# Performance work log

Measured on AMD Instinct MI355X. Metric: run time of the kernel, lower is better.

Reference implementation:

```python
import jax, jax.numpy as jnp
import numpy as np

DIM = 512
NUM_HEAD = 8
HEAD_DIM = DIM // NUM_HEAD
FFN = 4 * DIM


def setup_inputs() -> dict:
    key = jax.random.key(0)
    ks = jax.random.split(key, 16)
    s = DIM ** -0.5
    inp = {
        "x": jax.random.normal(ks[0], (4, 2048, DIM), jnp.float32),
        "wq": jax.random.normal(ks[1], (DIM, DIM), jnp.float32) * s,
        "bq": jnp.zeros((DIM,), jnp.float32),
        "wk": jax.random.normal(ks[2], (DIM, DIM), jnp.float32) * s,
        "bk": jnp.zeros((DIM,), jnp.float32),
        "wv": jax.random.normal(ks[3], (DIM, DIM), jnp.float32) * s,
        "bv": jnp.zeros((DIM,), jnp.float32),
        "wo": jax.random.normal(ks[4], (DIM, DIM), jnp.float32) * s,
        "bo": jnp.zeros((DIM,), jnp.float32),
        "w1": jax.random.normal(ks[5], (DIM, FFN), jnp.float32) * s,
        "b1": jnp.zeros((FFN,), jnp.float32),
        "w2": jax.random.normal(ks[6], (FFN, DIM), jnp.float32) * (FFN ** -0.5),
        "b2": jnp.zeros((DIM,), jnp.float32),
        "g1": jnp.ones((DIM,), jnp.float32),
        "be1": jnp.zeros((DIM,), jnp.float32),
        "g2": jnp.ones((DIM,), jnp.float32),
        "be2": jnp.zeros((DIM,), jnp.float32),
    }
    return inp


def layer_norm(x, g, b, eps=1e-5):
    mu = jnp.mean(x, axis=-1, keepdims=True)
    var = jnp.var(x, axis=-1, keepdims=True)
    return (x - mu) * jax.lax.rsqrt(var + eps) * g + b


def _forward(x, wq, bq, wk, bk, wv, bv, wo, bo, w1, b1, w2, b2, g1, be1, g2, be2):
    b, n, _ = x.shape
    scale = HEAD_DIM ** -0.5
    q = (x @ wq + bq).reshape(b, n, NUM_HEAD, HEAD_DIM).transpose(0, 2, 1, 3)
    k = (x @ wk + bk).reshape(b, n, NUM_HEAD, HEAD_DIM).transpose(0, 2, 1, 3)
    v = (x @ wv + bv).reshape(b, n, NUM_HEAD, HEAD_DIM).transpose(0, 2, 1, 3)
    scores = jnp.einsum('bhqd,bhkd->bhqk', q, k) * scale
    attn = jax.nn.softmax(scores, axis=-1)
    out = jnp.einsum('bhqk,bhkd->bhqd', attn, v)
    out = out.transpose(0, 2, 1, 3).reshape(b, n, DIM)
    out = out @ wo + bo
    x = layer_norm(out + x, g1, be1)
    h = jax.nn.gelu(x @ w1 + b1, approximate=False)
    ff = h @ w2 + b2
    x = layer_norm(ff + x, g2, be2)
    return x


def reference(x, wq, bq, wk, bk, wv, bv, wo, bo, w1, b1, w2, b2, g1, be1, g2, be2):
    return _forward(x, wq, bq, wk, bk, wv, bv, wo, bo, w1, b1, w2, b2, g1, be1, g2, be2)
```

## Files before the change

kernel.cpp:

```cpp
#include <hip/hip_runtime.h>
#include <math.h>

#define DIM 512
#define NHEAD 8
#define HD 64
#define FFN_DIM 2048
#define BATCH 4
#define SEQ 2048
#define MTOK (BATCH*SEQ)

typedef __attribute__((ext_vector_type(8))) short bf16x8;
typedef __attribute__((ext_vector_type(4))) float f32x4;

__device__ __forceinline__ unsigned short f2b(float f){
    unsigned int u = __float_as_uint(f);
    u += 0x7fffu + ((u >> 16) & 1u);
    return (unsigned short)(u >> 16);
}
__device__ __forceinline__ float b2f(unsigned short u){
    return __uint_as_float(((unsigned int)u) << 16);
}
__device__ __forceinline__ unsigned int pack_trunc(float f0, float f1){
    return __builtin_amdgcn_perm(__float_as_uint(f1), __float_as_uint(f0), 0x07060302u);
}
__device__ __forceinline__ void async_cp16(const unsigned short* g, unsigned short* l){
    __builtin_amdgcn_global_load_lds((const __attribute__((address_space(1))) unsigned int*)g,
                                     (__attribute__((address_space(3))) unsigned int*)l, 16, 0, 0);
}

__device__ __forceinline__ void transp32(const float* __restrict__ in, unsigned short* __restrict__ out,
                                         int N, int K, int n0_rd, int n0_wr, int k0,
                                         unsigned short (&t)[32][33], int tid){
    int tx = tid & 31, ty = tid >> 5;
    #pragma unroll
    for (int u = 0; u < 4; u++)
        t[tx][ty + 8*u] = f2b(in[(size_t)(k0 + ty + 8*u)*N + n0_rd + tx]);
    __syncthreads();
    #pragma unroll
    for (int u = 0; u < 4; u++)
        out[(size_t)(n0_wr + ty + 8*u)*K + k0 + tx] = t[ty + 8*u][tx];
}

__global__ void prep_kernel(const float* __restrict__ x,
                            const float* __restrict__ wq, const float* __restrict__ wk,
                            const float* __restrict__ wv, const float* __restrict__ wo,
                            const float* __restrict__ w1, const float* __restrict__ w2,
                            const float* __restrict__ bq, const float* __restrict__ bk,
                            const float* __restrict__ bv,
                            unsigned short* __restrict__ xb, unsigned short* __restrict__ wqkvT,
                            unsigned short* __restrict__ woT, unsigned short* __restrict__ w1T,
                            unsigned short* __restrict__ w2T, float* __restrict__ bqkv)
{
    __shared__ unsigned short t[32][33];
    int bid = blockIdx.x, tid = threadIdx.x;
    if (bid < 4096) {
        int i = (bid*256 + tid)*4;
        float4 v = *(const float4*)(x + i);
        ushort4 o; o.x=f2b(v.x); o.y=f2b(v.y); o.z=f2b(v.z); o.w=f2b(v.w);
        *(ushort4*)(xb + i) = o;
    } else if (bid < 4864) {
        int r = bid - 4096;
        int n0 = (r % 48)*32, k0 = (r / 48)*32;
        const float* w = (n0 < 512) ? wq : (n0 < 1024) ? wk : wv;
        transp32(w, wqkvT, 512, 512, n0 & 511, n0, k0, t, tid);
    } else if (bid < 5120) {
        int r = bid - 4864;
        int n0 = (r % 16)*32, k0 = (r / 16)*32;
        transp32(wo, woT, 512, 512, n0, n0, k0, t, tid);
    } else if (bid < 6144) {
        int r = bid - 5120;
        int n0 = (r % 64)*32, k0 = (r / 64)*32;
        transp32(w1, w1T, 2048, 512, n0, n0, k0, t, tid);
    } else if (bid < 7168) {
        int r = bid - 6144;
        int n0 = (r % 16)*32, k0 = (r / 16)*32;
        transp32(w2, w2T, 512, 2048, n0, n0, k0, t, tid);
    } else {
        int i = (bid - 7168)*256 + tid;
        if (i < 1536)
            bqkv[i] = (i < 512) ? bq[i] : (i < 1024) ? bk[i-512] : bv[i-1024];
    }
}

template<int MODE, int TN, int SK>
__global__ __launch_bounds__(256)
void gemm_bf16(const unsigned short* __restrict__ A, const unsigned short* __restrict__ Bt,
               const float* __restrict__ bias,
               float* __restrict__ Cf, unsigned short* __restrict__ Cb,
               unsigned short* __restrict__ qo, unsigned short* __restrict__ ko,
               unsigned short* __restrict__ vTo,
               int M, int N, int K)
{
    constexpr int JN = (TN == 128) ? 4 : 2;
    __shared__ unsigned short As[128*64];
    __shared__ unsigned short Bs[TN*64];
    int tid  = threadIdx.x;
    int lane = tid & 63;
    int ln = lane & 15, qd = lane >> 4;
    int m0 = blockIdx.x * 128, n0 = blockIdx.y * TN;
    int wid = tid >> 6;
    int wm = (wid >> 1) * 64;
    int wn = (wid & 1) * (16*JN);
    int kbeg = (SK > 1) ? (int)blockIdx.z * (K/SK) : 0;
    int kend = kbeg + K/SK;
    if (SK > 1) Cf += (size_t)blockIdx.z * M * N;

    f32x4 acc[4][JN];
    #pragma unroll
    for (int i = 0; i < 4; i++)
        #pragma unroll
        for (int j = 0; j < JN; j++) acc[i][j] = (f32x4){0.f,0.f,0.f,0.f};

    for (int k0 = kbeg; k0 < kend; k0 += 64) {
        #pragma unroll
        for (int i = 0; i < 4; i++) {
            int cid = i*256 + tid;
            int row = cid >> 3, cs = cid & 7;
            int cg = cs ^ (row & 7);
            async_cp16(&A[(size_t)(m0+row)*K + k0 + cg*8], &As[(cid & ~63) * 8]);
        }
        #pragma unroll
        for (int i = 0; i < TN/32; i++) {
            int cid = i*256 + tid;
            int row = cid >> 3, cs = cid & 7;
            int cg = cs ^ (row & 7);
            async_cp16(&Bt[(size_t)(n0+row)*K + k0 + cg*8], &Bs[(cid & ~63) * 8]);
        }
        __syncthreads();
        #pragma unroll
        for (int kk = 0; kk < 64; kk += 32) {
            int c0 = kk >> 3;
            bf16x8 af[4], bf[JN];
            #pragma unroll
            for (int t = 0; t < 4; t++)
                af[t] = *(bf16x8*)&As[(wm + t*16 + ln)*64 + ((c0 + qd) ^ (ln & 7))*8];
            #pragma unroll
            for (int t = 0; t < JN; t++)
                bf[t] = *(bf16x8*)&Bs[(wn + t*16 + ln)*64 + ((c0 + qd) ^ (ln & 7))*8];
            #pragma unroll
            for (int i = 0; i < 4; i++)
                #pragma unroll
                for (int j = 0; j < JN; j++)
                    acc[i][j] = __builtin_amdgcn_mfma_f32_16x16x32_bf16(af[i], bf[j], acc[i][j], 0,0,0);
        }
        __syncthreads();
    }

    const float QSCALE = 0.18033688011112042f;
    #pragma unroll
    for (int i = 0; i < 4; i++) {
        int mb = m0 + wm + i*16 + qd*4;
        #pragma unroll
        for (int j = 0; j < JN; j++) {
            int c = n0 + wn + j*16 + ln;
            float bv_ = (SK > 1 && blockIdx.z) ? 0.f : bias[c];
            float v[4];
            #pragma unroll
            for (int r = 0; r < 4; r++) v[r] = acc[i][j][r] + bv_;
            if (MODE == 0) {
                #pragma unroll
                for (int r = 0; r < 4; r++) Cf[(size_t)(mb+r)*N + c] = v[r];
            } else if (MODE == 2) {
                #pragma unroll
                for (int r = 0; r < 4; r++) {
                    float g = 0.5f * v[r] * (1.0f + erff(v[r] * 0.70710678118654752f));
                    Cb[(size_t)(mb+r)*N + c] = f2b(g);
                }
            } else {
                int b = mb >> 11, t0 = mb & 2047;
                if (c < 512) {
                    int h = c >> 6, hd = c & 63;
                    #pragma unroll
                    for (int r = 0; r < 4; r++)
                        qo[(((size_t)(b*8 + h))*SEQ + t0 + r)*64 + hd] = f2b(v[r] * QSCALE);
                } else if (c < 1024) {
                    int cc = c - 512, h = cc >> 6, hd = cc & 63;
                    #pragma unroll
                    for (int r = 0; r < 4; r++)
                        ko[(((size_t)(b*8 + h))*SEQ + t0 + r)*64 + hd] = f2b(v[r]);
                } else {
                    int cc = c - 1024, h = cc >> 6, hd = cc & 63;
                    ushort4 pk;
                    pk.x = f2b(v[0]); pk.y = f2b(v[1]); pk.z = f2b(v[2]); pk.w = f2b(v[3]);
                    *(ushort4*)&vTo[(((size_t)(b*8 + h))*64 + hd)*SEQ + t0] = pk;
                }
            }
        }
    }
}

__global__ __launch_bounds__(256)
void attn_mfma(const unsigned short* __restrict__ Q, const unsigned short* __restrict__ K,
               const unsigned short* __restrict__ VT, unsigned short* __restrict__ O)
{
    __shared__ unsigned short lds[24576];
    unsigned short* Qs = lds + 8192;
    unsigned short* Ps = lds + 16384;
    int tid  = threadIdx.x;
    int wid  = tid >> 6, lane = tid & 63;
    int ln = lane & 15, qd = lane >> 4;
    int qb = blockIdx.x, bh = blockIdx.y;

    #pragma unroll
    for (int i = 0; i < 4; i++) {
        int cid = i*256 + tid;
        int row = cid >> 3, cs = cid & 7;
        int cg = cs ^ (row & 7);
        async_cp16(&Q[((size_t)bh*SEQ + qb*128 + row)*64 + cg*8], &Qs[(cid & ~63)*8]);
    }
    #pragma unroll
    for (int i = 0; i < 2; i++) {
        int cid = i*256 + tid;
        int row = cid >> 3, cs = cid & 7;
        int cg = cs ^ (row & 7);
        async_cp16(&K [((size_t)bh*SEQ + row)*64 + cg*8], &lds[(cid & ~63)*8]);
        async_cp16(&VT[((size_t)bh*64 + row)*SEQ + cg*8], &lds[4096 + (cid & ~63)*8]);
    }
    __syncthreads();

    bf16x8 qf[2][2];
    #pragma unroll
    for (int qs = 0; qs < 2; qs++)
        #pragma unroll
        for (int kk = 0; kk < 2; kk++)
            qf[qs][kk] = *(bf16x8*)&Qs[(wid*32 + qs*16 + ln)*64 + ((kk*4 + qd) ^ (ln & 7))*8];
    __syncthreads();

    f32x4 o[2][4];
    #pragma unroll
    for (int qs = 0; qs < 2; qs++)
        #pragma unroll
        for (int dt = 0; dt < 4; dt++) o[qs][dt] = (f32x4){0.f,0.f,0.f,0.f};
    float l_i[2] = {0.f, 0.f};

    for (int kt = 0; kt < 32; kt++) {
        int kof = (kt & 1) * 8192;
        int vof = 4096 + kof;
        if (kt < 31) {
            int nkof = 8192 - kof;
            #pragma unroll
            for (int i = 0; i < 2; i++) {
                int cid = i*256 + tid;
                int row = cid >> 3, cs = cid & 7;
                int cg = cs ^ (row & 7);
                async_cp16(&K [((size_t)bh*SEQ + (kt+1)*64 + row)*64 + cg*8], &lds[nkof + (cid & ~63)*8]);
                async_cp16(&VT[((size_t)bh*64 + row)*SEQ + (kt+1)*64 + cg*8], &lds[nkof + 4096 + (cid & ~63)*8]);
            }
        }

        f32x4 s[2][4];
        #pragma unroll
        for (int qs = 0; qs < 2; qs++)
            #pragma unroll
            for (int nt = 0; nt < 4; nt++) s[qs][nt] = (f32x4){0.f,0.f,0.f,0.f};
        #pragma unroll
        for (int kk = 0; kk < 2; kk++) {
            #pragma unroll
            for (int nt = 0; nt < 4; nt++) {
                bf16x8 kf = *(bf16x8*)&lds[kof + (nt*16 + ln)*64 + ((kk*4 + qd) ^ (ln & 7))*8];
                s[0][nt] = __builtin_amdgcn_mfma_f32_16x16x32_bf16(kf, qf[0][kk], s[0][nt], 0,0,0);
                s[1][nt] = __builtin_amdgcn_mfma_f32_16x16x32_bf16(kf, qf[1][kk], s[1][nt], 0,0,0);
            }
        }

        #pragma unroll
        for (int qs = 0; qs < 2; qs++) {
            #pragma unroll
            for (int nt = 0; nt < 4; nt++) {
                #pragma unroll
                for (int r = 0; r < 4; r++) {
                    float p = __builtin_amdgcn_exp2f(s[qs][nt][r]);
                    s[qs][nt][r] = p;
                    l_i[qs] += p;
                }
                uint2 pk;
                pk.x = pack_trunc(s[qs][nt][0], s[qs][nt][1]);
                pk.y = pack_trunc(s[qs][nt][2], s[qs][nt][3]);
                *(uint2*)&Ps[(wid*32 + qs*16 + ln)*64 + ((nt*2 + (qd>>1)) ^ (ln & 7))*8 + (qd&1)*4] = pk;
            }
        }

        #pragma unroll
        for (int kk = 0; kk < 2; kk++) {
            bf16x8 pf0 = *(bf16x8*)&Ps[(wid*32 + ln)*64      + ((kk*4 + qd) ^ (ln & 7))*8];
            bf16x8 pf1 = *(bf16x8*)&Ps[(wid*32 + 16 + ln)*64 + ((kk*4 + qd) ^ (ln & 7))*8];
            #pragma unroll
            for (int dt = 0; dt < 4; dt++) {
                bf16x8 vf = *(bf16x8*)&lds[vof + (dt*16 + ln)*64 + ((kk*4 + qd) ^ (ln & 7))*8];
                o[0][dt] = __builtin_amdgcn_mfma_f32_16x16x32_bf16(vf, pf0, o[0][dt], 0,0,0);
                o[1][dt] = __builtin_amdgcn_mfma_f32_16x16x32_bf16(vf, pf1, o[1][dt], 0,0,0);
            }
        }
        __syncthreads();
    }

    int b = bh >> 3, h = bh & 7;
    #pragma unroll
    for (int qs = 0; qs < 2; qs++) {
        float l = l_i[qs];
        l += __shfl_xor(l, 16);
        l += __shfl_xor(l, 32);
        float linv = 1.0f / l;
        int t = qb*128 + wid*32 + qs*16 + ln;
        #pragma unroll
        for (int dt = 0; dt < 4; dt++) {
            ushort4 pk;
            pk.x = f2b(o[qs][dt][0]*linv); pk.y = f2b(o[qs][dt][1]*linv);
            pk.z = f2b(o[qs][dt][2]*linv); pk.w = f2b(o[qs][dt][3]*linv);
            *(ushort4*)&O[((size_t)b*SEQ + t)*DIM + h*64 + dt*16 + qd*4] = pk;
        }
    }
}

__global__ void ln1_kernel(const float* __restrict__ m0p, const float* __restrict__ m1p,
                           const float* __restrict__ resp,
                           const float* __restrict__ g, const float* __restrict__ be,
                           unsigned short* __restrict__ outb)
{
    int row  = blockIdx.x*4 + (threadIdx.x >> 6);
    int lane = threadIdx.x & 63;
    size_t base = (size_t)row * DIM + lane*8;

    float4 a0 = *(const float4*)(m0p + base);
    float4 a1 = *(const float4*)(m0p + base + 4);
    float4 c0 = *(const float4*)(m1p + base);
    float4 c1 = *(const float4*)(m1p + base + 4);
    float4 r0 = *(const float4*)(resp + base);
    float4 r1 = *(const float4*)(resp + base + 4);
    float v[8] = { a0.x+c0.x+r0.x, a0.y+c0.y+r0.y, a0.z+c0.z+r0.z, a0.w+c0.w+r0.w,
                   a1.x+c1.x+r1.x, a1.y+c1.y+r1.y, a1.z+c1.z+r1.z, a1.w+c1.w+r1.w };
    float s = 0.f, s2 = 0.f;
    #pragma unroll
    for (int i = 0; i < 8; i++) { s += v[i]; s2 += v[i]*v[i]; }
    #pragma unroll
    for (int d = 32; d >= 1; d >>= 1) { s += __shfl_xor(s, d); s2 += __shfl_xor(s2, d); }
    float mean = s * (1.0f / DIM);
    float rstd = rsqrtf(s2 * (1.0f / DIM) - mean*mean + 1e-5f);

    float4 g0 = *(const float4*)(g + lane*8);
    float4 g1 = *(const float4*)(g + lane*8 + 4);
    float4 b0 = *(const float4*)(be + lane*8);
    float4 b1 = *(const float4*)(be + lane*8 + 4);
    float gg[8] = {g0.x,g0.y,g0.z,g0.w,g1.x,g1.y,g1.z,g1.w};
    float bb[8] = {b0.x,b0.y,b0.z,b0.w,b1.x,b1.y,b1.z,b1.w};
    ushort4 p0, p1;
    float o[8];
    #pragma unroll
    for (int i = 0; i < 8; i++) o[i] = (v[i]-mean)*rstd*gg[i] + bb[i];
    p0.x=f2b(o[0]); p0.y=f2b(o[1]); p0.z=f2b(o[2]); p0.w=f2b(o[3]);
    p1.x=f2b(o[4]); p1.y=f2b(o[5]); p1.z=f2b(o[6]); p1.w=f2b(o[7]);
    *(ushort4*)(outb + base)     = p0;
    *(ushort4*)(outb + base + 4) = p1;
}

__global__ void ln2_kernel(const float* __restrict__ m0p, const float* __restrict__ m1p,
                           const unsigned short* __restrict__ resb,
                           const float* __restrict__ g, const float* __restrict__ be,
                           float* __restrict__ outf)
{
    int row  = blockIdx.x*4 + (threadIdx.x >> 6);
    int lane = threadIdx.x & 63;
    size_t base = (size_t)row * DIM + lane*8;

    float4 a0 = *(const float4*)(m0p + base);
    float4 a1 = *(const float4*)(m0p + base + 4);
    float4 c0 = *(const float4*)(m1p + base);
    float4 c1 = *(const float4*)(m1p + base + 4);
    ushort4 rb0 = *(const ushort4*)(resb + base);
    ushort4 rb1 = *(const ushort4*)(resb + base + 4);
    float v[8] = { a0.x+c0.x+b2f(rb0.x), a0.y+c0.y+b2f(rb0.y),
                   a0.z+c0.z+b2f(rb0.z), a0.w+c0.w+b2f(rb0.w),
                   a1.x+c1.x+b2f(rb1.x), a1.y+c1.y+b2f(rb1.y),
                   a1.z+c1.z+b2f(rb1.z), a1.w+c1.w+b2f(rb1.w) };
    float s = 0.f, s2 = 0.f;
    #pragma unroll
    for (int i = 0; i < 8; i++) { s += v[i]; s2 += v[i]*v[i]; }
    #pragma unroll
    for (int d = 32; d >= 1; d >>= 1) { s += __shfl_xor(s, d); s2 += __shfl_xor(s2, d); }
    float mean = s * (1.0f / DIM);
    float rstd = rsqrtf(s2 * (1.0f / DIM) - mean*mean + 1e-5f);

    float4 g0 = *(const float4*)(g + lane*8);
    float4 g1 = *(const float4*)(g + lane*8 + 4);
    float4 b0 = *(const float4*)(be + lane*8);
    float4 b1 = *(const float4*)(be + lane*8 + 4);
    float gg[8] = {g0.x,g0.y,g0.z,g0.w,g1.x,g1.y,g1.z,g1.w};
    float bb[8] = {b0.x,b0.y,b0.z,b0.w,b1.x,b1.y,b1.z,b1.w};
    float o[8];
    #pragma unroll
    for (int i = 0; i < 8; i++) o[i] = (v[i] - mean)*rstd*gg[i] + bb[i];
    *(float4*)(outf + base)     = (float4){o[0],o[1],o[2],o[3]};
    *(float4*)(outf + base + 4) = (float4){o[4],o[5],o[6],o[7]};
}

extern "C" void kernel_launch(void* const* d_in, const int* in_sizes, int n_in,
                              void* d_out, int out_size, void* d_ws, size_t ws_size,
                              hipStream_t stream) {
    const float* x   = (const float*)d_in[0];
    const float* wq  = (const float*)d_in[1];
    const float* bq  = (const float*)d_in[2];
    const float* wk  = (const float*)d_in[3];
    const float* bk  = (const float*)d_in[4];
    const float* wv  = (const float*)d_in[5];
    const float* bv  = (const float*)d_in[6];
    const float* wo  = (const float*)d_in[7];
    const float* bo  = (const float*)d_in[8];
    const float* w1  = (const float*)d_in[9];
    const float* b1  = (const float*)d_in[10];
    const float* w2  = (const float*)d_in[11];
    const float* b2  = (const float*)d_in[12];
    const float* g1  = (const float*)d_in[13];
    const float* be1 = (const float*)d_in[14];
    const float* g2  = (const float*)d_in[15];
    const float* be2 = (const float*)d_in[16];
    float* out = (float*)d_out;

    char* w = (char*)d_ws;
    size_t off = 0;
    auto alloc = [&](size_t bytes){ void* p = w + off; off += (bytes + 255) & ~(size_t)255; return p; };
    unsigned short* xb     = (unsigned short*)alloc((size_t)MTOK*DIM*2);
    unsigned short* wqkvT  = (unsigned short*)alloc((size_t)1536*512*2);
    unsigned short* woT    = (unsigned short*)alloc((size_t)512*512*2);
    unsigned short* w1T    = (unsigned short*)alloc((size_t)2048*512*2);
    unsigned short* w2T    = (unsigned short*)alloc((size_t)512*2048*2);
    float*          bqkv   = (float*)alloc(1536*4);
    unsigned short* qb_    = (unsigned short*)alloc((size_t)32*SEQ*64*2);
    unsigned short* kb_    = (unsigned short*)alloc((size_t)32*SEQ*64*2);
    unsigned short* vT_    = (unsigned short*)alloc((size_t)32*64*SEQ*2);
    unsigned short* attno  = (unsigned short*)alloc((size_t)MTOK*DIM*2);
    unsigned short* x1b    = (unsigned short*)alloc((size_t)MTOK*DIM*2);
    unsigned short* h_     = (unsigned short*)alloc((size_t)MTOK*FFN_DIM*2);
    float*          ff     = (float*)alloc((size_t)2*MTOK*DIM*4);

    prep_kernel<<<7174, 256, 0, stream>>>(x, wq, wk, wv, wo, w1, w2, bq, bk, bv,
                                          xb, wqkvT, woT, w1T, w2T, bqkv);

    gemm_bf16<1,128,1><<<dim3(64,12), 256, 0, stream>>>(xb, wqkvT, bqkv, nullptr, nullptr,
                                                        qb_, kb_, vT_, MTOK, 1536, DIM);
    attn_mfma<<<dim3(16,32), 256, 0, stream>>>(qb_, kb_, vT_, attno);
    gemm_bf16<0,128,2><<<dim3(64,4,2), 256, 0, stream>>>(attno, woT, bo, ff, nullptr,
                                                         nullptr, nullptr, nullptr, MTOK, DIM, DIM);
    ln1_kernel<<<MTOK/4, 256, 0, stream>>>(ff, ff + (size_t)MTOK*DIM, x, g1, be1, x1b);
    gemm_bf16<2,128,1><<<dim3(64,16), 256, 0, stream>>>(x1b, w1T, b1, nullptr, h_,
                                                        nullptr, nullptr, nullptr, MTOK, FFN_DIM, DIM);
    gemm_bf16<0,128,2><<<dim3(64,4,2), 256, 0, stream>>>(h_, w2T, b2, ff, nullptr,
                                                         nullptr, nullptr, nullptr, MTOK, DIM, FFN_DIM);
    ln2_kernel<<<MTOK/4, 256, 0, stream>>>(ff, ff + (size_t)MTOK*DIM, x1b, g2, be2, out);
}
```

Measured before the change: 272.4 us.

## Use two-wave attention blocks with 64 rows per wave; bf16 split-K partials

Attention blocks now use 128 threads, each wave handling 64 query rows, so every K/V fragment read from LDS feeds twice as many MFMAs. The Q tile is staged in the P buffer region. Split-K GEMM partial outputs feeding the layer norms are stored in bf16 rather than fp32, halving that write/read traffic. This costs more registers per wave and adds bf16 rounding before the residual and layer norm.

```diff
diff --git a/kernel.cpp b/kernel.cpp
--- a/kernel.cpp
+++ b/kernel.cpp
@@ -86,7 +86,7 @@
 __global__ __launch_bounds__(256)
 void gemm_bf16(const unsigned short* __restrict__ A, const unsigned short* __restrict__ Bt,
                const float* __restrict__ bias,
-               float* __restrict__ Cf, unsigned short* __restrict__ Cb,
+               unsigned short* __restrict__ Cb,
                unsigned short* __restrict__ qo, unsigned short* __restrict__ ko,
                unsigned short* __restrict__ vTo,
                int M, int N, int K)
@@ -103,7 +103,7 @@
     int wn = (wid & 1) * (16*JN);
     int kbeg = (SK > 1) ? (int)blockIdx.z * (K/SK) : 0;
     int kend = kbeg + K/SK;
-    if (SK > 1) Cf += (size_t)blockIdx.z * M * N;
+    if (SK > 1 && MODE == 0) Cb += (size_t)blockIdx.z * M * N;
 
     f32x4 acc[4][JN];
     #pragma unroll
@@ -159,7 +159,7 @@
             for (int r = 0; r < 4; r++) v[r] = acc[i][j][r] + bv_;
             if (MODE == 0) {
                 #pragma unroll
-                for (int r = 0; r < 4; r++) Cf[(size_t)(mb+r)*N + c] = v[r];
+                for (int r = 0; r < 4; r++) Cb[(size_t)(mb+r)*N + c] = f2b(v[r]);
             } else if (MODE == 2) {
                 #pragma unroll
                 for (int r = 0; r < 4; r++) {
@@ -189,12 +189,11 @@
     }
 }
 
-__global__ __launch_bounds__(256)
+__global__ __launch_bounds__(128)
 void attn_mfma(const unsigned short* __restrict__ Q, const unsigned short* __restrict__ K,
                const unsigned short* __restrict__ VT, unsigned short* __restrict__ O)
 {
     __shared__ unsigned short lds[24576];
-    unsigned short* Qs = lds + 8192;
     unsigned short* Ps = lds + 16384;
     int tid  = threadIdx.x;
     int wid  = tid >> 6, lane = tid & 63;
@@ -202,15 +201,15 @@
     int qb = blockIdx.x, bh = blockIdx.y;
 
     #pragma unroll
-    for (int i = 0; i < 4; i++) {
-        int cid = i*256 + tid;
+    for (int i = 0; i < 8; i++) {
+        int cid = i*128 + tid;
         int row = cid >> 3, cs = cid & 7;
         int cg = cs ^ (row & 7);
-        async_cp16(&Q[((size_t)bh*SEQ + qb*128 + row)*64 + cg*8], &Qs[(cid & ~63)*8]);
-    }
-    #pragma unroll
-    for (int i = 0; i < 2; i++) {
-        int cid = i*256 + tid;
+        async_cp16(&Q[((size_t)bh*SEQ + qb*128 + row)*64 + cg*8], &Ps[(cid & ~63)*8]);
+    }
+    #pragma unroll
+    for (int i = 0; i < 4; i++) {
+        int cid = i*128 + tid;
         int row = cid >> 3, cs = cid & 7;
         int cg = cs ^ (row & 7);
         async_cp16(&K [((size_t)bh*SEQ + row)*64 + cg*8], &lds[(cid & ~63)*8]);
@@ -218,20 +217,20 @@
     }
     __syncthreads();
 
-    bf16x8 qf[2][2];
-    #pragma unroll
-    for (int qs = 0; qs < 2; qs++)
+    bf16x8 qf[4][2];
+    #pragma unroll
+    for (int qs = 0; qs < 4; qs++)
         #pragma unroll
         for (int kk = 0; kk < 2; kk++)
-            qf[qs][kk] = *(bf16x8*)&Qs[(wid*32 + qs*16 + ln)*64 + ((kk*4 + qd) ^ (ln & 7))*8];
+            qf[qs][kk] = *(bf16x8*)&Ps[(wid*64 + qs*16 + ln)*64 + ((kk*4 + qd) ^ (ln & 7))*8];
     __syncthreads();
 
-    f32x4 o[2][4];
-    #pragma unroll
-    for (int qs = 0; qs < 2; qs++)
+    f32x4 o[4][4];
+    #pragma unroll
+    for (int qs = 0; qs < 4; qs++)
         #pragma unroll
         for (int dt = 0; dt < 4; dt++) o[qs][dt] = (f32x4){0.f,0.f,0.f,0.f};
-    float l_i[2] = {0.f, 0.f};
+    float l_i[4] = {0.f, 0.f, 0.f, 0.f};
 
     for (int kt = 0; kt < 32; kt++) {
         int kof = (kt & 1) * 8192;
@@ -239,8 +238,8 @@
         if (kt < 31) {
             int nkof = 8192 - kof;
             #pragma unroll
-            for (int i = 0; i < 2; i++) {
-                int cid = i*256 + tid;
+            for (int i = 0; i < 4; i++) {
+                int cid = i*128 + tid;
                 int row = cid >> 3, cs = cid & 7;
                 int cg = cs ^ (row & 7);
                 async_cp16(&K [((size_t)bh*SEQ + (kt+1)*64 + row)*64 + cg*8], &lds[nkof + (cid & ~63)*8]);
@@ -248,9 +247,9 @@
             }
         }
 
-        f32x4 s[2][4];
-        #pragma unroll
-        for (int qs = 0; qs < 2; qs++)
+        f32x4 s[4][4];
+        #pragma unroll
+        for (int qs = 0; qs < 4; qs++)
             #pragma unroll
             for (int nt = 0; nt < 4; nt++) s[qs][nt] = (f32x4){0.f,0.f,0.f,0.f};
         #pragma unroll
@@ -258,13 +257,14 @@
             #pragma unroll
             for (int nt = 0; nt < 4; nt++) {
                 bf16x8 kf = *(bf16x8*)&lds[kof + (nt*16 + ln)*64 + ((kk*4 + qd) ^ (ln & 7))*8];
-                s[0][nt] = __builtin_amdgcn_mfma_f32_16x16x32_bf16(kf, qf[0][kk], s[0][nt], 0,0,0);
-                s[1][nt] = __builtin_amdgcn_mfma_f32_16x16x32_bf16(kf, qf[1][kk], s[1][nt], 0,0,0);
+                #pragma unroll
+                for (int qs = 0; qs < 4; qs++)
+                    s[qs][nt] = __builtin_amdgcn_mfma_f32_16x16x32_bf16(kf, qf[qs][kk], s[qs][nt], 0,0,0);
             }
         }
 
         #pragma unroll
-        for (int qs = 0; qs < 2; qs++) {
+        for (int qs = 0; qs < 4; qs++) {
             #pragma unroll
             for (int nt = 0; nt < 4; nt++) {
                 #pragma unroll
@@ -276,19 +276,22 @@
                 uint2 pk;
                 pk.x = pack_trunc(s[qs][nt][0], s[qs][nt][1]);
                 pk.y = pack_trunc(s[qs][nt][2], s[qs][nt][3]);
-                *(uint2*)&Ps[(wid*32 + qs*16 + ln)*64 + ((nt*2 + (qd>>1)) ^ (ln & 7))*8 + (qd&1)*4] = pk;
+                *(uint2*)&Ps[(wid*64 + qs*16 + ln)*64 + ((nt*2 + (qd>>1)) ^ (ln & 7))*8 + (qd&1)*4] = pk;
             }
         }
 
         #pragma unroll
         for (int kk = 0; kk < 2; kk++) {
-            bf16x8 pf0 = *(bf16x8*)&Ps[(wid*32 + ln)*64      + ((kk*4 + qd) ^ (ln & 7))*8];
-            bf16x8 pf1 = *(bf16x8*)&Ps[(wid*32 + 16 + ln)*64 + ((kk*4 + qd) ^ (ln & 7))*8];
+            bf16x8 pf[4];
+            #pragma unroll
+            for (int qs = 0; qs < 4; qs++)
+                pf[qs] = *(bf16x8*)&Ps[(wid*64 + qs*16 + ln)*64 + ((kk*4 + qd) ^ (ln & 7))*8];
             #pragma unroll
             for (int dt = 0; dt < 4; dt++) {
                 bf16x8 vf = *(bf16x8*)&lds[vof + (dt*16 + ln)*64 + ((kk*4 + qd) ^ (ln & 7))*8];
-                o[0][dt] = __builtin_amdgcn_mfma_f32_16x16x32_bf16(vf, pf0, o[0][dt], 0,0,0);
-                o[1][dt] = __builtin_amdgcn_mfma_f32_16x16x32_bf16(vf, pf1, o[1][dt], 0,0,0);
+                #pragma unroll
+                for (int qs = 0; qs < 4; qs++)
+                    o[qs][dt] = __builtin_amdgcn_mfma_f32_16x16x32_bf16(vf, pf[qs], o[qs][dt], 0,0,0);
             }
         }
         __syncthreads();
@@ -296,12 +299,12 @@
 
     int b = bh >> 3, h = bh & 7;
     #pragma unroll
-    for (int qs = 0; qs < 2; qs++) {
+    for (int qs = 0; qs < 4; qs++) {
         float l = l_i[qs];
         l += __shfl_xor(l, 16);
         l += __shfl_xor(l, 32);
         float linv = 1.0f / l;
-        int t = qb*128 + wid*32 + qs*16 + ln;
+        int t = qb*128 + wid*64 + qs*16 + ln;
         #pragma unroll
         for (int dt = 0; dt < 4; dt++) {
             ushort4 pk;
@@ -312,7 +315,7 @@
     }
 }
 
-__global__ void ln1_kernel(const float* __restrict__ m0p, const float* __restrict__ m1p,
+__global__ void ln1_kernel(const unsigned short* __restrict__ m0b, const unsigned short* __restrict__ m1b,
                            const float* __restrict__ resp,
                            const float* __restrict__ g, const float* __restrict__ be,
                            unsigned short* __restrict__ outb)
@@ -321,14 +324,16 @@
     int lane = threadIdx.x & 63;
     size_t base = (size_t)row * DIM + lane*8;
 
-    float4 a0 = *(const float4*)(m0p + base);
-    float4 a1 = *(const float4*)(m0p + base + 4);
-    float4 c0 = *(const float4*)(m1p + base);
-    float4 c1 = *(const float4*)(m1p + base + 4);
+    ushort4 a0 = *(const ushort4*)(m0b + base);
+    ushort4 a1 = *(const ushort4*)(m0b + base + 4);
+    ushort4 c0 = *(const ushort4*)(m1b + base);
+    ushort4 c1 = *(const ushort4*)(m1b + base + 4);
     float4 r0 = *(const float4*)(resp + base);
     float4 r1 = *(const float4*)(resp + base + 4);
-    float v[8] = { a0.x+c0.x+r0.x, a0.y+c0.y+r0.y, a0.z+c0.z+r0.z, a0.w+c0.w+r0.w,
-                   a1.x+c1.x+r1.x, a1.y+c1.y+r1.y, a1.z+c1.z+r1.z, a1.w+c1.w+r1.w };
+    float v[8] = { b2f(a0.x)+b2f(c0.x)+r0.x, b2f(a0.y)+b2f(c0.y)+r0.y,
+                   b2f(a0.z)+b2f(c0.z)+r0.z, b2f(a0.w)+b2f(c0.w)+r0.w,
+                   b2f(a1.x)+b2f(c1.x)+r1.x, b2f(a1.y)+b2f(c1.y)+r1.y,
+                   b2f(a1.z)+b2f(c1.z)+r1.z, b2f(a1.w)+b2f(c1.w)+r1.w };
     float s = 0.f, s2 = 0.f;
     #pragma unroll
     for (int i = 0; i < 8; i++) { s += v[i]; s2 += v[i]*v[i]; }
@@ -343,17 +348,17 @@
     float4 b1 = *(const float4*)(be + lane*8 + 4);
     float gg[8] = {g0.x,g0.y,g0.z,g0.w,g1.x,g1.y,g1.z,g1.w};
     float bb[8] = {b0.x,b0.y,b0.z,b0.w,b1.x,b1.y,b1.z,b1.w};
+    float o[8];
+    #pragma unroll
+    for (int i = 0; i < 8; i++) o[i] = (v[i]-mean)*rstd*gg[i] + bb[i];
     ushort4 p0, p1;
-    float o[8];
-    #pragma unroll
-    for (int i = 0; i < 8; i++) o[i] = (v[i]-mean)*rstd*gg[i] + bb[i];
     p0.x=f2b(o[0]); p0.y=f2b(o[1]); p0.z=f2b(o[2]); p0.w=f2b(o[3]);
     p1.x=f2b(o[4]); p1.y=f2b(o[5]); p1.z=f2b(o[6]); p1.w=f2b(o[7]);
     *(ushort4*)(outb + base)     = p0;
     *(ushort4*)(outb + base + 4) = p1;
 }
 
-__global__ void ln2_kernel(const float* __restrict__ m0p, const float* __restrict__ m1p,
+__global__ void ln2_kernel(const unsigned short* __restrict__ m0b, const unsigned short* __restrict__ m1b,
                            const unsigned short* __restrict__ resb,
                            const float* __restrict__ g, const float* __restrict__ be,
                            float* __restrict__ outf)
@@ -362,16 +367,16 @@
     int lane = threadIdx.x & 63;
     size_t base = (size_t)row * DIM + lane*8;
 
-    float4 a0 = *(const float4*)(m0p + base);
-    float4 a1 = *(const float4*)(m0p + base + 4);
-    float4 c0 = *(const float4*)(m1p + base);
-    float4 c1 = *(const float4*)(m1p + base + 4);
+    ushort4 a0 = *(const ushort4*)(m0b + base);
+    ushort4 a1 = *(const ushort4*)(m0b + base + 4);
+    ushort4 c0 = *(const ushort4*)(m1b + base);
+    ushort4 c1 = *(const ushort4*)(m1b + base + 4);
     ushort4 rb0 = *(const ushort4*)(resb + base);
     ushort4 rb1 = *(const ushort4*)(resb + base + 4);
-    float v[8] = { a0.x+c0.x+b2f(rb0.x), a0.y+c0.y+b2f(rb0.y),
-                   a0.z+c0.z+b2f(rb0.z), a0.w+c0.w+b2f(rb0.w),
-                   a1.x+c1.x+b2f(rb1.x), a1.y+c1.y+b2f(rb1.y),
-                   a1.z+c1.z+b2f(rb1.z), a1.w+c1.w+b2f(rb1.w) };
+    float v[8] = { b2f(a0.x)+b2f(c0.x)+b2f(rb0.x), b2f(a0.y)+b2f(c0.y)+b2f(rb0.y),
+                   b2f(a0.z)+b2f(c0.z)+b2f(rb0.z), b2f(a0.w)+b2f(c0.w)+b2f(rb0.w),
+                   b2f(a1.x)+b2f(c1.x)+b2f(rb1.x), b2f(a1.y)+b2f(c1.y)+b2f(rb1.y),
+                   b2f(a1.z)+b2f(c1.z)+b2f(rb1.z), b2f(a1.w)+b2f(c1.w)+b2f(rb1.w) };
     float s = 0.f, s2 = 0.f;
     #pragma unroll
     for (int i = 0; i < 8; i++) { s += v[i]; s2 += v[i]*v[i]; }
@@ -430,20 +435,20 @@
     unsigned short* attno  = (unsigned short*)alloc((size_t)MTOK*DIM*2);
     unsigned short* x1b    = (unsigned short*)alloc((size_t)MTOK*DIM*2);
     unsigned short* h_     = (unsigned short*)alloc((size_t)MTOK*FFN_DIM*2);
-    float*          ff     = (float*)alloc((size_t)2*MTOK*DIM*4);
+    unsigned short* ffb    = (unsigned short*)alloc((size_t)2*MTOK*DIM*2);
 
     prep_kernel<<<7174, 256, 0, stream>>>(x, wq, wk, wv, wo, w1, w2, bq, bk, bv,
                                           xb, wqkvT, woT, w1T, w2T, bqkv);
 
-    gemm_bf16<1,128,1><<<dim3(64,12), 256, 0, stream>>>(xb, wqkvT, bqkv, nullptr, nullptr,
+    gemm_bf16<1,128,1><<<dim3(64,12), 256, 0, stream>>>(xb, wqkvT, bqkv, nullptr,
                                                         qb_, kb_, vT_, MTOK, 1536, DIM);
-    attn_mfma<<<dim3(16,32), 256, 0, stream>>>(qb_, kb_, vT_, attno);
-    gemm_bf16<0,128,2><<<dim3(64,4,2), 256, 0, stream>>>(attno, woT, bo, ff, nullptr,
+    attn_mfma<<<dim3(16,32), 128, 0, stream>>>(qb_, kb_, vT_, attno);
+    gemm_bf16<0,128,2><<<dim3(64,4,2), 256, 0, stream>>>(attno, woT, bo, ffb,
                                                          nullptr, nullptr, nullptr, MTOK, DIM, DIM);
-    ln1_kernel<<<MTOK/4, 256, 0, stream>>>(ff, ff + (size_t)MTOK*DIM, x, g1, be1, x1b);
-    gemm_bf16<2,128,1><<<dim3(64,16), 256, 0, stream>>>(x1b, w1T, b1, nullptr, h_,
+    ln1_kernel<<<MTOK/4, 256, 0, stream>>>(ffb, ffb + (size_t)MTOK*DIM, x, g1, be1, x1b);
+    gemm_bf16<2,128,1><<<dim3(64,16), 256, 0, stream>>>(x1b, w1T, b1, h_,
                                                         nullptr, nullptr, nullptr, MTOK, FFN_DIM, DIM);
-    gemm_bf16<0,128,2><<<dim3(64,4,2), 256, 0, stream>>>(h_, w2T, b2, ff, nullptr,
+    gemm_bf16<0,128,2><<<dim3(64,4,2), 256, 0, stream>>>(h_, w2T, b2, ffb,
                                                          nullptr, nullptr, nullptr, MTOK, DIM, FFN_DIM);
-    ln2_kernel<<<MTOK/4, 256, 0, stream>>>(ff, ff + (size_t)MTOK*DIM, x1b, g2, be2, out);
-}
+    ln2_kernel<<<MTOK/4, 256, 0, stream>>>(ffb, ffb + (size_t)MTOK*DIM, x1b, g2, be2, out);
+}
```

Measured after the change: 276.3 us. About the same (+1.5%).

## Use larger GEMM tiles, 4-way split-K for FFN2, and bf16 partial outputs

Applied to the files above, without the earlier changes.

Generalizes the GEMM template to TM/TN tile sizes with 8 accumulator columns per wave when a tile dimension is 256. The W1 GEMM now uses 128x256 tiles and the W2 GEMM uses 256x128 tiles with 4-way split-K. Split-K partial sums are stored as bf16 instead of fp32, and the layernorm kernels read and add the bf16 partials (four for ln2). This is meant to improve data reuse and cut partial-sum traffic, at the cost of lower precision in the residual partials and higher register pressure.

```diff
diff --git a/kernel.cpp b/kernel.cpp
--- a/kernel.cpp
+++ b/kernel.cpp
@@ -82,28 +82,30 @@
     }
 }
 
-template<int MODE, int TN, int SK>
+template<int MODE, int TM, int TN, int SK>
 __global__ __launch_bounds__(256)
 void gemm_bf16(const unsigned short* __restrict__ A, const unsigned short* __restrict__ Bt,
                const float* __restrict__ bias,
-               float* __restrict__ Cf, unsigned short* __restrict__ Cb,
+               unsigned short* __restrict__ Cb,
                unsigned short* __restrict__ qo, unsigned short* __restrict__ ko,
                unsigned short* __restrict__ vTo,
                int M, int N, int K)
 {
-    constexpr int JN = (TN == 128) ? 4 : 2;
-    __shared__ unsigned short As[128*64];
+    constexpr int JN = (TM == 256 || TN == 256) ? 8 : 4;
+    __shared__ unsigned short As[TM*64];
     __shared__ unsigned short Bs[TN*64];
     int tid  = threadIdx.x;
     int lane = tid & 63;
     int ln = lane & 15, qd = lane >> 4;
-    int m0 = blockIdx.x * 128, n0 = blockIdx.y * TN;
+    int m0 = blockIdx.x * TM, n0 = blockIdx.y * TN;
     int wid = tid >> 6;
-    int wm = (wid >> 1) * 64;
-    int wn = (wid & 1) * (16*JN);
+    int wm, wn;
+    if (TM == 256)      { wm = wid*64;        wn = 0; }
+    else if (TN == 256) { wm = (wid >> 1)*64; wn = (wid & 1)*128; }
+    else                { wm = (wid >> 1)*64; wn = (wid & 1)*64; }
     int kbeg = (SK > 1) ? (int)blockIdx.z * (K/SK) : 0;
     int kend = kbeg + K/SK;
-    if (SK > 1) Cf += (size_t)blockIdx.z * M * N;
+    if (SK > 1 && MODE == 0) Cb += (size_t)blockIdx.z * M * N;
 
     f32x4 acc[4][JN];
     #pragma unroll
@@ -113,7 +115,7 @@
 
     for (int k0 = kbeg; k0 < kend; k0 += 64) {
         #pragma unroll
-        for (int i = 0; i < 4; i++) {
+        for (int i = 0; i < TM/32; i++) {
             int cid = i*256 + tid;
             int row = cid >> 3, cs = cid & 7;
             int cg = cs ^ (row & 7);
@@ -159,7 +161,7 @@
             for (int r = 0; r < 4; r++) v[r] = acc[i][j][r] + bv_;
             if (MODE == 0) {
                 #pragma unroll
-                for (int r = 0; r < 4; r++) Cf[(size_t)(mb+r)*N + c] = v[r];
+                for (int r = 0; r < 4; r++) Cb[(size_t)(mb+r)*N + c] = f2b(v[r]);
             } else if (MODE == 2) {
                 #pragma unroll
                 for (int r = 0; r < 4; r++) {
@@ -312,7 +314,7 @@
     }
 }
 
-__global__ void ln1_kernel(const float* __restrict__ m0p, const float* __restrict__ m1p,
+__global__ void ln1_kernel(const unsigned short* __restrict__ m0b, const unsigned short* __restrict__ m1b,
                            const float* __restrict__ resp,
                            const float* __restrict__ g, const float* __restrict__ be,
                            unsigned short* __restrict__ outb)
@@ -321,14 +323,16 @@
     int lane = threadIdx.x & 63;
     size_t base = (size_t)row * DIM + lane*8;
 
-    float4 a0 = *(const float4*)(m0p + base);
-    float4 a1 = *(const float4*)(m0p + base + 4);
-    float4 c0 = *(const float4*)(m1p + base);
-    float4 c1 = *(const float4*)(m1p + base + 4);
+    ushort4 a0 = *(const ushort4*)(m0b + base);
+    ushort4 a1 = *(const ushort4*)(m0b + base + 4);
+    ushort4 c0 = *(const ushort4*)(m1b + base);
+    ushort4 c1 = *(const ushort4*)(m1b + base + 4);
     float4 r0 = *(const float4*)(resp + base);
     float4 r1 = *(const float4*)(resp + base + 4);
-    float v[8] = { a0.x+c0.x+r0.x, a0.y+c0.y+r0.y, a0.z+c0.z+r0.z, a0.w+c0.w+r0.w,
-                   a1.x+c1.x+r1.x, a1.y+c1.y+r1.y, a1.z+c1.z+r1.z, a1.w+c1.w+r1.w };
+    float v[8] = { b2f(a0.x)+b2f(c0.x)+r0.x, b2f(a0.y)+b2f(c0.y)+r0.y,
+                   b2f(a0.z)+b2f(c0.z)+r0.z, b2f(a0.w)+b2f(c0.w)+r0.w,
+                   b2f(a1.x)+b2f(c1.x)+r1.x, b2f(a1.y)+b2f(c1.y)+r1.y,
+                   b2f(a1.z)+b2f(c1.z)+r1.z, b2f(a1.w)+b2f(c1.w)+r1.w };
     float s = 0.f, s2 = 0.f;
     #pragma unroll
     for (int i = 0; i < 8; i++) { s += v[i]; s2 += v[i]*v[i]; }
@@ -343,17 +347,17 @@
     float4 b1 = *(const float4*)(be + lane*8 + 4);
     float gg[8] = {g0.x,g0.y,g0.z,g0.w,g1.x,g1.y,g1.z,g1.w};
     float bb[8] = {b0.x,b0.y,b0.z,b0.w,b1.x,b1.y,b1.z,b1.w};
+    float o[8];
+    #pragma unroll
+    for (int i = 0; i < 8; i++) o[i] = (v[i]-mean)*rstd*gg[i] + bb[i];
     ushort4 p0, p1;
-    float o[8];
-    #pragma unroll
-    for (int i = 0; i < 8; i++) o[i] = (v[i]-mean)*rstd*gg[i] + bb[i];
     p0.x=f2b(o[0]); p0.y=f2b(o[1]); p0.z=f2b(o[2]); p0.w=f2b(o[3]);
     p1.x=f2b(o[4]); p1.y=f2b(o[5]); p1.z=f2b(o[6]); p1.w=f2b(o[7]);
     *(ushort4*)(outb + base)     = p0;
     *(ushort4*)(outb + base + 4) = p1;
 }
 
-__global__ void ln2_kernel(const float* __restrict__ m0p, const float* __restrict__ m1p,
+__global__ void ln2_kernel(const unsigned short* __restrict__ mb,
                            const unsigned short* __restrict__ resb,
                            const float* __restrict__ g, const float* __restrict__ be,
                            float* __restrict__ outf)
@@ -361,17 +365,22 @@
     int row  = blockIdx.x*4 + (threadIdx.x >> 6);
     int lane = threadIdx.x & 63;
     size_t base = (size_t)row * DIM + lane*8;
-
-    float4 a0 = *(const float4*)(m0p + base);
-    float4 a1 = *(const float4*)(m0p + base + 4);
-    float4 c0 = *(const float4*)(m1p + base);
-    float4 c1 = *(const float4*)(m1p + base + 4);
-    ushort4 rb0 = *(const ushort4*)(resb + base);
-    ushort4 rb1 = *(const ushort4*)(resb + base + 4);
-    float v[8] = { a0.x+c0.x+b2f(rb0.x), a0.y+c0.y+b2f(rb0.y),
-                   a0.z+c0.z+b2f(rb0.z), a0.w+c0.w+b2f(rb0.w),
-                   a1.x+c1.x+b2f(rb1.x), a1.y+c1.y+b2f(rb1.y),
-                   a1.z+c1.z+b2f(rb1.z), a1.w+c1.w+b2f(rb1.w) };
+    const size_t PSTRIDE = (size_t)MTOK * DIM;
+
+    float v[8];
+    {
+        ushort4 rb0 = *(const ushort4*)(resb + base);
+        ushort4 rb1 = *(const ushort4*)(resb + base + 4);
+        v[0]=b2f(rb0.x); v[1]=b2f(rb0.y); v[2]=b2f(rb0.z); v[3]=b2f(rb0.w);
+        v[4]=b2f(rb1.x); v[5]=b2f(rb1.y); v[6]=b2f(rb1.z); v[7]=b2f(rb1.w);
+    }
+    #pragma unroll
+    for (int p = 0; p < 4; p++) {
+        ushort4 a0 = *(const ushort4*)(mb + p*PSTRIDE + base);
+        ushort4 a1 = *(const ushort4*)(mb + p*PSTRIDE + base + 4);
+        v[0]+=b2f(a0.x); v[1]+=b2f(a0.y); v[2]+=b2f(a0.z); v[3]+=b2f(a0.w);
+        v[4]+=b2f(a1.x); v[5]+=b2f(a1.y); v[6]+=b2f(a1.z); v[7]+=b2f(a1.w);
+    }
     float s = 0.f, s2 = 0.f;
     #pragma unroll
     for (int i = 0; i < 8; i++) { s += v[i]; s2 += v[i]*v[i]; }
@@ -430,20 +439,20 @@
     unsigned short* attno  = (unsigned short*)alloc((size_t)MTOK*DIM*2);
     unsigned short* x1b    = (unsigned short*)alloc((size_t)MTOK*DIM*2);
     unsigned short* h_     = (unsigned short*)alloc((size_t)MTOK*FFN_DIM*2);
-    float*          ff     = (float*)alloc((size_t)2*MTOK*DIM*4);
+    unsigned short* ffb    = (unsigned short*)alloc((size_t)4*MTOK*DIM*2);
 
     prep_kernel<<<7174, 256, 0, stream>>>(x, wq, wk, wv, wo, w1, w2, bq, bk, bv,
                                           xb, wqkvT, woT, w1T, w2T, bqkv);
 
-    gemm_bf16<1,128,1><<<dim3(64,12), 256, 0, stream>>>(xb, wqkvT, bqkv, nullptr, nullptr,
-                                                        qb_, kb_, vT_, MTOK, 1536, DIM);
+    gemm_bf16<1,128,128,1><<<dim3(64,12), 256, 0, stream>>>(xb, wqkvT, bqkv, nullptr,
+                                                            qb_, kb_, vT_, MTOK, 1536, DIM);
     attn_mfma<<<dim3(16,32), 256, 0, stream>>>(qb_, kb_, vT_, attno);
-    gemm_bf16<0,128,2><<<dim3(64,4,2), 256, 0, stream>>>(attno, woT, bo, ff, nullptr,
-                                                         nullptr, nullptr, nullptr, MTOK, DIM, DIM);
-    ln1_kernel<<<MTOK/4, 256, 0, stream>>>(ff, ff + (size_t)MTOK*DIM, x, g1, be1, x1b);
-    gemm_bf16<2,128,1><<<dim3(64,16), 256, 0, stream>>>(x1b, w1T, b1, nullptr, h_,
-                                                        nullptr, nullptr, nullptr, MTOK, FFN_DIM, DIM);
-    gemm_bf16<0,128,2><<<dim3(64,4,2), 256, 0, stream>>>(h_, w2T, b2, ff, nullptr,
-                                                         nullptr, nullptr, nullptr, MTOK, DIM, FFN_DIM);
-    ln2_kernel<<<MTOK/4, 256, 0, stream>>>(ff, ff + (size_t)MTOK*DIM, x1b, g2, be2, out);
-}
+    gemm_bf16<0,128,128,2><<<dim3(64,4,2), 256, 0, stream>>>(attno, woT, bo, ffb,
+                                                             nullptr, nullptr, nullptr, MTOK, DIM, DIM);
+    ln1_kernel<<<MTOK/4, 256, 0, stream>>>(ffb, ffb + (size_t)MTOK*DIM, x, g1, be1, x1b);
+    gemm_bf16<2,128,256,1><<<dim3(64,8), 256, 0, stream>>>(x1b, w1T, b1, h_,
+                                                           nullptr, nullptr, nullptr, MTOK, FFN_DIM, DIM);
+    gemm_bf16<0,256,128,4><<<dim3(32,4,4), 256, 0, stream>>>(h_, w2T, b2, ffb,
+                                                             nullptr, nullptr, nullptr, MTOK, DIM, FFN_DIM);
+    ln2_kernel<<<MTOK/4, 256, 0, stream>>>(ffb, x1b, g2, be2, out);
+}
```

After: 322.0 us. 1.18x slower.
